# Performance work log

Hardware: AMD Instinct MI355X
Metric: run time of the kernel (lower is better)

## Reference

```python
import jax, jax.numpy as jnp
import numpy as np

HIDDEN = 1024
HEADS = 16
HEAD_DIM = HIDDEN // HEADS


def setup_inputs() -> dict:
    key = jax.random.key(0)
    ks = jax.random.split(key, 9)
    s = 1.0 / np.sqrt(HIDDEN)
    x = jax.random.normal(ks[0], (1, 4096, HIDDEN), dtype=jnp.float32)
    return {
        "x": x,
        "wq": jax.random.normal(ks[1], (HIDDEN, HIDDEN), dtype=jnp.float32) * s,
        "bq": jnp.zeros((HIDDEN,), dtype=jnp.float32),
        "wk": jax.random.normal(ks[2], (HIDDEN, HIDDEN), dtype=jnp.float32) * s,
        "bk": jnp.zeros((HIDDEN,), dtype=jnp.float32),
        "wv": jax.random.normal(ks[3], (HIDDEN, HIDDEN), dtype=jnp.float32) * s,
        "bv": jnp.zeros((HIDDEN,), dtype=jnp.float32),
        "wo": jax.random.normal(ks[4], (HIDDEN, HIDDEN), dtype=jnp.float32) * s,
        "bo": jnp.zeros((HIDDEN,), dtype=jnp.float32),
    }


def reference(x, wq, bq, wk, bk, wv, bv, wo, bo):
    B, S, D = x.shape
    H, Hd = HEADS, HEAD_DIM
    # projections (torch Linear: y = x @ W.T + b)
    q = (x @ wq.T + bq).reshape(B, S, H, Hd).transpose(0, 2, 1, 3)  # [B,H,S,Hd]
    k = (x @ wk.T + bk).reshape(B, S, H, Hd).transpose(0, 2, 1, 3)
    v = (x @ wv.T + bv).reshape(B, S, H, Hd).transpose(0, 2, 1, 3)
    scores = jnp.einsum("bhqd,bhkd->bhqk", q, k) / jnp.sqrt(jnp.float32(Hd))
    attn = jax.nn.softmax(scores, axis=-1)  # full [B,H,S,S] matrix, faithful to source
    out = jnp.einsum("bhqk,bhkd->bhqd", attn, v)  # [B,H,S,Hd]
    out = out.transpose(0, 2, 1, 3).reshape(B, S, D)
    return out @ wo.T + bo
```

## Files before the change

### kernel.cpp

```cpp
#include <hip/hip_runtime.h>
#include <stdint.h>

#define S 4096
#define D 1024
#define H 16
#define HD 64

#define QK_SCALE 0.18033688011112042f

typedef short short8  __attribute__((ext_vector_type(8)));
typedef float floatx4 __attribute__((ext_vector_type(4)));
typedef float floatx16 __attribute__((ext_vector_type(16)));

__device__ __forceinline__ unsigned short f2bf(float f) {
  union { float f; unsigned int i; } x; x.f = f;
  unsigned int r = x.i + 0x7FFFu + ((x.i >> 16) & 1u);
  return (unsigned short)(r >> 16);
}

#if defined(__has_builtin)
#if __has_builtin(__builtin_amdgcn_cvt_pk_bf16_f32)
#define HAVE_PK_BF16 1
#endif
#if __has_builtin(__builtin_amdgcn_exp2f)
#define HAVE_RAW_EXP2 1
#endif
#endif

__device__ __forceinline__ unsigned int pkbf(float a, float b) {
#ifdef HAVE_PK_BF16
  typedef __bf16 bf2_t __attribute__((ext_vector_type(2)));
  bf2_t t = __builtin_amdgcn_cvt_pk_bf16_f32(a, b);
  return __builtin_bit_cast(unsigned int, t);
#else
  return (unsigned int)f2bf(a) | ((unsigned int)f2bf(b) << 16);
#endif
}

__device__ __forceinline__ float fexp2(float x) {
#ifdef HAVE_RAW_EXP2
  return __builtin_amdgcn_exp2f(x);
#else
  return exp2f(x);
#endif
}

__device__ __forceinline__ void async16(const unsigned short* g, unsigned short* l) {
  __builtin_amdgcn_global_load_lds(
      (const __attribute__((address_space(1))) unsigned int*)g,
      (__attribute__((address_space(3))) unsigned int*)l, 16, 0, 0);
}

__global__ __launch_bounds__(256) void cvt_kernel(
    const float* __restrict__ x,  unsigned short* __restrict__ xb,
    const float* __restrict__ wq, unsigned short* __restrict__ wqb,
    const float* __restrict__ wk, unsigned short* __restrict__ wkb,
    const float* __restrict__ wv, unsigned short* __restrict__ wvb,
    const float* __restrict__ wo, unsigned short* __restrict__ wob,
    const float* __restrict__ bq, float* __restrict__ bqs)
{
  const int z = blockIdx.y;
  const float* s; unsigned short* d;
  float scale = 1.f;
  if (z < 4)       { s = x + (size_t)z * 1048576; d = xb + (size_t)z * 1048576; }
  else if (z == 4) { s = wq; d = wqb; scale = QK_SCALE; }
  else if (z == 5) { s = wk; d = wkb; }
  else if (z == 6) { s = wv; d = wvb; }
  else             { s = wo; d = wob; }
  const size_t i = ((size_t)blockIdx.x * 256 + threadIdx.x) * 4;
  float4 v = *reinterpret_cast<const float4*>(s + i);
  uint2 o;
  o.x = pkbf(v.x * scale, v.y * scale);
  o.y = pkbf(v.z * scale, v.w * scale);
  *reinterpret_cast<uint2*>(d + i) = o;
  if (z == 4 && blockIdx.x == 0) {
    const int t = threadIdx.x;
    #pragma unroll
    for (int j = 0; j < 4; ++j) bqs[t * 4 + j] = bq[t * 4 + j] * QK_SCALE;
  }
}

__global__ __launch_bounds__(256) void gemm_bt(
    const unsigned short* __restrict__ X,
    const unsigned short* __restrict__ W0, const float* __restrict__ B0, unsigned short* __restrict__ C0,
    const unsigned short* __restrict__ W1, const float* __restrict__ B1, unsigned short* __restrict__ C1,
    const unsigned short* __restrict__ W2, const float* __restrict__ B2, unsigned short* __restrict__ C2,
    float* __restrict__ Cf, unsigned short* __restrict__ VtOut)
{
  const unsigned short* W; const float* Bb; unsigned short* C;
  const int z = blockIdx.z;
  if (z == 0)      { W = W0; Bb = B0; C = C0; }
  else if (z == 1) { W = W1; Bb = B1; C = C1; }
  else             { W = W2; Bb = B2; C = C2; }

  const int bm = blockIdx.y, bn = blockIdx.x;
  const int tid  = threadIdx.x;
  const int lane = tid & 63, wave = tid >> 6;
  const int quad = lane >> 4, n16 = lane & 15;
  const int wm = (wave >> 1) * 64, wn = (wave & 1) * 64;

  __shared__ union {
    struct { unsigned short A[2][128 * 32]; unsigned short B[2][128 * 32]; } s;
    unsigned short T[64 * 136];
  } sm;

  floatx4 zero = {0.f, 0.f, 0.f, 0.f};
  floatx4 acc[4][4];
  #pragma unroll
  for (int i = 0; i < 4; ++i)
    #pragma unroll
    for (int j = 0; j < 4; ++j) acc[i][j] = zero;

  const int srow = 16 * wave + (lane >> 2);
  const int scol = (lane & 3) * 8;
  const unsigned short* XaL = X + (size_t)(bm * 128 + srow) * D + scol;
  const unsigned short* WaL = W + (size_t)(bn * 128 + srow) * D + scol;
  unsigned short* ldsA[2][2], * ldsB[2][2];
  #pragma unroll
  for (int sl = 0; sl < 2; ++sl) {
    ldsA[sl][0] = &sm.s.A[sl][(16 * wave) * 32];
    ldsA[sl][1] = &sm.s.A[sl][(64 + 16 * wave) * 32];
    ldsB[sl][0] = &sm.s.B[sl][(16 * wave) * 32];
    ldsB[sl][1] = &sm.s.B[sl][(64 + 16 * wave) * 32];
  }

  for (int k0 = 0; k0 < D; k0 += 64) {
    __syncthreads();
    #pragma unroll
    for (int sl = 0; sl < 2; ++sl) {
      async16(XaL + k0 + sl * 32, ldsA[sl][0]);
      async16(XaL + (size_t)64 * D + k0 + sl * 32, ldsA[sl][1]);
      async16(WaL + k0 + sl * 32, ldsB[sl][0]);
      async16(WaL + (size_t)64 * D + k0 + sl * 32, ldsB[sl][1]);
    }
    __syncthreads();

    #pragma unroll
    for (int sl = 0; sl < 2; ++sl) {
      short8 af[4], bfr[4];
      #pragma unroll
      for (int t = 0; t < 4; ++t) {
        af[t]  = *reinterpret_cast<const short8*>(&sm.s.A[sl][(wm + t * 16 + n16) * 32 + quad * 8]);
        bfr[t] = *reinterpret_cast<const short8*>(&sm.s.B[sl][(wn + t * 16 + n16) * 32 + quad * 8]);
      }
      #pragma unroll
      for (int tm = 0; tm < 4; ++tm)
        #pragma unroll
        for (int tn = 0; tn < 4; ++tn)
          acc[tm][tn] = __builtin_amdgcn_mfma_f32_16x16x32_bf16(af[tm], bfr[tn], acc[tm][tn], 0, 0, 0);
    }
  }

  if (z == 2 && VtOut) {
    #pragma unroll
    for (int p = 0; p < 2; ++p) {
      __syncthreads();
      if ((wn >> 6) == p) {
        #pragma unroll
        for (int tn = 0; tn < 4; ++tn) {
          const int col = bn * 128 + p * 64 + tn * 16 + n16;
          const float bias = Bb[col];
          #pragma unroll
          for (int tm = 0; tm < 4; ++tm) {
            uint2 w;
            w.x = pkbf(acc[tm][tn][0] + bias, acc[tm][tn][1] + bias);
            w.y = pkbf(acc[tm][tn][2] + bias, acc[tm][tn][3] + bias);
            *reinterpret_cast<uint2*>(&sm.T[(tn * 16 + n16) * 136 + wm + tm * 16 + quad * 4]) = w;
          }
        }
      }
      __syncthreads();
      {
        const int rl = tid >> 2, cc = (tid & 3) * 32;
        uint4 t0 = *reinterpret_cast<const uint4*>(&sm.T[rl * 136 + cc]);
        uint4 t1 = *reinterpret_cast<const uint4*>(&sm.T[rl * 136 + cc + 8]);
        uint4 t2 = *reinterpret_cast<const uint4*>(&sm.T[rl * 136 + cc + 16]);
        uint4 t3 = *reinterpret_cast<const uint4*>(&sm.T[rl * 136 + cc + 24]);
        uint4 n0, n1, n2, n3;
        n0.x = t0.x; n0.y = t0.y; n0.z = t1.x; n0.w = t1.y;
        n1.x = t0.z; n1.y = t0.w; n1.z = t1.z; n1.w = t1.w;
        n2.x = t2.x; n2.y = t2.y; n2.z = t3.x; n2.w = t3.y;
        n3.x = t2.z; n3.y = t2.w; n3.z = t3.z; n3.w = t3.w;
        const size_t go = (size_t)(bn * 128 + p * 64 + rl) * S + bm * 128 + cc;
        *reinterpret_cast<uint4*>(&VtOut[go])      = n0;
        *reinterpret_cast<uint4*>(&VtOut[go + 8])  = n1;
        *reinterpret_cast<uint4*>(&VtOut[go + 16]) = n2;
        *reinterpret_cast<uint4*>(&VtOut[go + 24]) = n3;
      }
    }
    return;
  }

  #pragma unroll
  for (int tn = 0; tn < 4; ++tn) {
    const int col = bn * 128 + wn + tn * 16 + n16;
    const float bias = Bb[col];
    #pragma unroll
    for (int tm = 0; tm < 4; ++tm) {
      const int rowb = bm * 128 + wm + tm * 16 + quad * 4;
      #pragma unroll
      for (int r = 0; r < 4; ++r) {
        const float v = acc[tm][tn][r] + bias;
        if (Cf) Cf[(size_t)(rowb + r) * D + col] = v;
        else    C[(size_t)(rowb + r) * D + col]  = f2bf(v);
      }
    }
  }
}

__global__ __launch_bounds__(256, 2) void attn(
    const unsigned short* __restrict__ Q,
    const unsigned short* __restrict__ K,
    const unsigned short* __restrict__ Vt,
    unsigned short* __restrict__ Op,
    float* __restrict__ Ls)
{
  const int h    = blockIdx.y;
  const int z    = blockIdx.z;
  const int q0   = blockIdx.x * 256;
  const int key0 = z * (S / 2);
  const int tid  = threadIdx.x;
  const int lane = tid & 63, wave = tid >> 6;
  const int l31 = lane & 31, h8 = lane >> 5;

  __shared__ unsigned short Ks[64 * 72];
  __shared__ unsigned short Vs[64 * 72];

  const int qA = q0 + wave * 64 + l31;
  const int qB = qA + 32;
  short8 qfA[4], qfB[4];
  #pragma unroll
  for (int ks = 0; ks < 4; ++ks) {
    qfA[ks] = *reinterpret_cast<const short8*>(Q + (size_t)qA * D + h * HD + ks * 16 + h8 * 8);
    qfB[ks] = *reinterpret_cast<const short8*>(Q + (size_t)qB * D + h * HD + ks * 16 + h8 * 8);
  }

  const short ONE = (short)0x3F80;
  short8 ones = {ONE, ONE, ONE, ONE, ONE, ONE, ONE, ONE};

  floatx16 oA0 = {}, oA1 = {}, oB0 = {}, oB1 = {};
  floatx16 accSA = {}, accSB = {};

  const int r1 = tid >> 2, c16 = (tid & 3) * 16;
  const unsigned short* Kbase = K  + (size_t)(key0 + r1) * D + h * HD + c16;
  const unsigned short* Vbase = Vt + (size_t)(h * HD + r1) * S + key0 + c16;

  uint4 ka, kb, va, vb;
  ka = *reinterpret_cast<const uint4*>(Kbase);
  kb = *reinterpret_cast<const uint4*>(Kbase + 8);
  va = *reinterpret_cast<const uint4*>(Vbase);
  vb = *reinterpret_cast<const uint4*>(Vbase + 8);

  const int NIT = (S / 2) / 64;
  for (int kt = 0; kt < NIT; ++kt) {
    __syncthreads();
    *reinterpret_cast<uint4*>(&Ks[r1 * 72 + c16])     = ka;
    *reinterpret_cast<uint4*>(&Ks[r1 * 72 + c16 + 8]) = kb;
    *reinterpret_cast<uint4*>(&Vs[r1 * 72 + c16])     = va;
    *reinterpret_cast<uint4*>(&Vs[r1 * 72 + c16 + 8]) = vb;
    __syncthreads();

    const int kn = (kt < NIT - 1) ? kt + 1 : kt;
    ka = *reinterpret_cast<const uint4*>(Kbase + (size_t)kn * 64 * D);
    kb = *reinterpret_cast<const uint4*>(Kbase + (size_t)kn * 64 * D + 8);
    va = *reinterpret_cast<const uint4*>(Vbase + kn * 64);
    vb = *reinterpret_cast<const uint4*>(Vbase + kn * 64 + 8);

    floatx16 sA0 = {}, sA1 = {}, sB0 = {}, sB1 = {};
    #pragma unroll
    for (int ks = 0; ks < 4; ++ks) {
      short8 a0 = *reinterpret_cast<const short8*>(&Ks[l31 * 72 + ks * 16 + h8 * 8]);
      short8 a1 = *reinterpret_cast<const short8*>(&Ks[(32 + l31) * 72 + ks * 16 + h8 * 8]);
      sA0 = __builtin_amdgcn_mfma_f32_32x32x16_bf16(a0, qfA[ks], sA0, 0, 0, 0);
      sA1 = __builtin_amdgcn_mfma_f32_32x32x16_bf16(a1, qfA[ks], sA1, 0, 0, 0);
      sB0 = __builtin_amdgcn_mfma_f32_32x32x16_bf16(a0, qfB[ks], sB0, 0, 0, 0);
      sB1 = __builtin_amdgcn_mfma_f32_32x32x16_bf16(a1, qfB[ks], sB1, 0, 0, 0);
    }

    #pragma unroll
    for (int r = 0; r < 16; ++r) {
      sA0[r] = fexp2(sA0[r]);
      sA1[r] = fexp2(sA1[r]);
      sB0[r] = fexp2(sB0[r]);
      sB1[r] = fexp2(sB1[r]);
    }

    short8 pbA[4], pbB[4];
    {
      unsigned int* ua = reinterpret_cast<unsigned int*>(pbA);
      unsigned int* ub = reinterpret_cast<unsigned int*>(pbB);
      #pragma unroll
      for (int i = 0; i < 8; ++i) {
        ua[i]     = pkbf(sA0[2 * i], sA0[2 * i + 1]);
        ua[8 + i] = pkbf(sA1[2 * i], sA1[2 * i + 1]);
        ub[i]     = pkbf(sB0[2 * i], sB0[2 * i + 1]);
        ub[8 + i] = pkbf(sB1[2 * i], sB1[2 * i + 1]);
      }
    }

    #pragma unroll
    for (int ks = 0; ks < 4; ++ks) {
      short8 va0 = *reinterpret_cast<const short8*>(&Vs[l31 * 72 + ks * 16 + h8 * 8]);
      short8 va1 = *reinterpret_cast<const short8*>(&Vs[(32 + l31) * 72 + ks * 16 + h8 * 8]);
      oA0 = __builtin_amdgcn_mfma_f32_32x32x16_bf16(va0, pbA[ks], oA0, 0, 0, 0);
      oA1 = __builtin_amdgcn_mfma_f32_32x32x16_bf16(va1, pbA[ks], oA1, 0, 0, 0);
      oB0 = __builtin_amdgcn_mfma_f32_32x32x16_bf16(va0, pbB[ks], oB0, 0, 0, 0);
      oB1 = __builtin_amdgcn_mfma_f32_32x32x16_bf16(va1, pbB[ks], oB1, 0, 0, 0);
      accSA = __builtin_amdgcn_mfma_f32_32x32x16_bf16(ones, pbA[ks], accSA, 0, 0, 0);
      accSB = __builtin_amdgcn_mfma_f32_32x32x16_bf16(ones, pbB[ks], accSB, 0, 0, 0);
    }
  }

  if (h8 == 0) {
    Ls[(size_t)z * S * H + qA * H + h] = accSA[0];
    Ls[(size_t)z * S * H + qB * H + h] = accSB[0];
  }

  unsigned short* obA = Op + (size_t)z * S * D + (size_t)qA * D + h * HD;
  unsigned short* obB = Op + (size_t)z * S * D + (size_t)qB * D + h * HD;
  #pragma unroll
  for (int rg = 0; rg < 4; ++rg) {
    uint2 w0, w1;
    w0.x = pkbf(oA0[rg * 4 + 0], oA0[rg * 4 + 1]);
    w0.y = pkbf(oA0[rg * 4 + 2], oA0[rg * 4 + 3]);
    w1.x = pkbf(oA1[rg * 4 + 0], oA1[rg * 4 + 1]);
    w1.y = pkbf(oA1[rg * 4 + 2], oA1[rg * 4 + 3]);
    *reinterpret_cast<uint2*>(&obA[rg * 8 + h8 * 4])      = w0;
    *reinterpret_cast<uint2*>(&obA[32 + rg * 8 + h8 * 4]) = w1;
    uint2 v0, v1;
    v0.x = pkbf(oB0[rg * 4 + 0], oB0[rg * 4 + 1]);
    v0.y = pkbf(oB0[rg * 4 + 2], oB0[rg * 4 + 3]);
    v1.x = pkbf(oB1[rg * 4 + 0], oB1[rg * 4 + 1]);
    v1.y = pkbf(oB1[rg * 4 + 2], oB1[rg * 4 + 3]);
    *reinterpret_cast<uint2*>(&obB[rg * 8 + h8 * 4])      = v0;
    *reinterpret_cast<uint2*>(&obB[32 + rg * 8 + h8 * 4]) = v1;
  }
}

__global__ __launch_bounds__(256) void combine(
    unsigned short* __restrict__ Op,
    const float* __restrict__ Ls)
{
  const size_t e8 = ((size_t)blockIdx.x * 256 + threadIdx.x) * 8;
  const int q = (int)(e8 >> 10);
  const int col = (int)(e8 & 1023);
  const int hh = col >> 6;
  const float l = Ls[q * H + hh] + Ls[S * H + q * H + hh];
  const float inv = 1.f / l;
  uint4 a = *reinterpret_cast<const uint4*>(Op + e8);
  uint4 b = *reinterpret_cast<const uint4*>(Op + (size_t)S * D + e8);
  uint4 r;
  const unsigned int* au = &a.x; const unsigned int* bu = &b.x; unsigned int* ru = &r.x;
  #pragma unroll
  for (int w = 0; w < 4; ++w) {
    union { unsigned int i; float f; } alo, ahi, blo, bhi;
    alo.i = au[w] << 16;          ahi.i = au[w] & 0xFFFF0000u;
    blo.i = bu[w] << 16;          bhi.i = bu[w] & 0xFFFF0000u;
    ru[w] = pkbf((alo.f + blo.f) * inv, (ahi.f + bhi.f) * inv);
  }
  *reinterpret_cast<uint4*>(Op + e8) = r;
}

extern "C" void kernel_launch(void* const* d_in, const int* in_sizes, int n_in,
                              void* d_out, int out_size, void* d_ws, size_t ws_size,
                              hipStream_t stream) {
  const float* x  = (const float*)d_in[0];
  const float* wq = (const float*)d_in[1];
  const float* bq = (const float*)d_in[2];
  const float* wk = (const float*)d_in[3];
  const float* bk = (const float*)d_in[4];
  const float* wv = (const float*)d_in[5];
  const float* bv = (const float*)d_in[6];
  const float* wo = (const float*)d_in[7];
  const float* bo = (const float*)d_in[8];
  float* out = (float*)d_out;

  unsigned short* ws = (unsigned short*)d_ws;
  const size_t SD = (size_t)S * D;
  const size_t DD = (size_t)D * D;
  unsigned short* xb  = ws;
  unsigned short* wqb = xb + SD;
  unsigned short* wkb = wqb + DD;
  unsigned short* wvb = wkb + DD;
  unsigned short* wob = wvb + DD;
  unsigned short* Qw  = wob + DD;
  unsigned short* Kw  = Qw + SD;
  unsigned short* Vtw = Kw + SD;
  unsigned short* Op  = Vtw + SD;
  float* Ls  = (float*)(Op + 2 * SD);
  float* bqs = Ls + 2 * (size_t)S * H;

  dim3 blk(256);
  cvt_kernel<<<dim3(1024, 8), blk, 0, stream>>>(x, xb, wq, wqb, wk, wkb, wv, wvb, wo, wob, bq, bqs);
  gemm_bt<<<dim3(D / 128, S / 128, 3), blk, 0, stream>>>(
      xb, wqb, bqs, Qw, wkb, bk, Kw, wvb, bv, nullptr, nullptr, Vtw);
  attn<<<dim3(S / 256, H, 2), blk, 0, stream>>>(Qw, Kw, Vtw, Op, Ls);
  combine<<<dim3(SD / (256 * 8)), blk, 0, stream>>>(Op, Ls);
  gemm_bt<<<dim3(D / 128, S / 128, 1), blk, 0, stream>>>(
      Op, wob, bo, nullptr, wob, bo, nullptr, wob, bo, nullptr, out, nullptr);
}
```

Baseline: 251.6 us.

## Fuse split-KV combine into output projection GEMM with 64-row tiles

Result: slower. 267.1 us (+6.2%).

```diff
diff --git a/kernel.cpp b/kernel.cpp
--- a/kernel.cpp
+++ b/kernel.cpp
@@ -43,6 +43,13 @@
 #else
   return exp2f(x);
 #endif
+}
+
+__device__ __forceinline__ unsigned int addpk(unsigned int a, unsigned int b, float inv) {
+  union { unsigned int i; float f; } alo, ahi, blo, bhi;
+  alo.i = a << 16;  ahi.i = a & 0xFFFF0000u;
+  blo.i = b << 16;  bhi.i = b & 0xFFFF0000u;
+  return pkbf((alo.f + blo.f) * inv, (ahi.f + bhi.f) * inv);
 }
 
 __device__ __forceinline__ void async16(const unsigned short* g, unsigned short* l) {
@@ -85,7 +92,7 @@
     const unsigned short* __restrict__ W0, const float* __restrict__ B0, unsigned short* __restrict__ C0,
     const unsigned short* __restrict__ W1, const float* __restrict__ B1, unsigned short* __restrict__ C1,
     const unsigned short* __restrict__ W2, const float* __restrict__ B2, unsigned short* __restrict__ C2,
-    float* __restrict__ Cf, unsigned short* __restrict__ VtOut)
+    unsigned short* __restrict__ VtOut)
 {
   const unsigned short* W; const float* Bb; unsigned short* C;
   const int z = blockIdx.z;
@@ -104,34 +111,21 @@
     unsigned short T[64 * 136];
   } sm;
 
-  floatx4 zero = {0.f, 0.f, 0.f, 0.f};
-  floatx4 acc[4][4];
-  #pragma unroll
-  for (int i = 0; i < 4; ++i)
-    #pragma unroll
-    for (int j = 0; j < 4; ++j) acc[i][j] = zero;
+  floatx4 acc[4][4] = {};
 
   const int srow = 16 * wave + (lane >> 2);
   const int scol = (lane & 3) * 8;
   const unsigned short* XaL = X + (size_t)(bm * 128 + srow) * D + scol;
   const unsigned short* WaL = W + (size_t)(bn * 128 + srow) * D + scol;
-  unsigned short* ldsA[2][2], * ldsB[2][2];
-  #pragma unroll
-  for (int sl = 0; sl < 2; ++sl) {
-    ldsA[sl][0] = &sm.s.A[sl][(16 * wave) * 32];
-    ldsA[sl][1] = &sm.s.A[sl][(64 + 16 * wave) * 32];
-    ldsB[sl][0] = &sm.s.B[sl][(16 * wave) * 32];
-    ldsB[sl][1] = &sm.s.B[sl][(64 + 16 * wave) * 32];
-  }
 
   for (int k0 = 0; k0 < D; k0 += 64) {
     __syncthreads();
     #pragma unroll
     for (int sl = 0; sl < 2; ++sl) {
-      async16(XaL + k0 + sl * 32, ldsA[sl][0]);
-      async16(XaL + (size_t)64 * D + k0 + sl * 32, ldsA[sl][1]);
-      async16(WaL + k0 + sl * 32, ldsB[sl][0]);
-      async16(WaL + (size_t)64 * D + k0 + sl * 32, ldsB[sl][1]);
+      async16(XaL + k0 + sl * 32, &sm.s.A[sl][(16 * wave) * 32]);
+      async16(XaL + (size_t)64 * D + k0 + sl * 32, &sm.s.A[sl][(64 + 16 * wave) * 32]);
+      async16(WaL + k0 + sl * 32, &sm.s.B[sl][(16 * wave) * 32]);
+      async16(WaL + (size_t)64 * D + k0 + sl * 32, &sm.s.B[sl][(64 + 16 * wave) * 32]);
     }
     __syncthreads();
 
@@ -199,11 +193,8 @@
     for (int tm = 0; tm < 4; ++tm) {
       const int rowb = bm * 128 + wm + tm * 16 + quad * 4;
       #pragma unroll
-      for (int r = 0; r < 4; ++r) {
-        const float v = acc[tm][tn][r] + bias;
-        if (Cf) Cf[(size_t)(rowb + r) * D + col] = v;
-        else    C[(size_t)(rowb + r) * D + col]  = f2bf(v);
-      }
+      for (int r = 0; r < 4; ++r)
+        C[(size_t)(rowb + r) * D + col] = f2bf(acc[tm][tn][r] + bias);
     }
   }
 }
@@ -337,28 +328,76 @@
   }
 }
 
-__global__ __launch_bounds__(256) void combine(
-    unsigned short* __restrict__ Op,
-    const float* __restrict__ Ls)
+__global__ __launch_bounds__(256) void gemm_out64(
+    const unsigned short* __restrict__ Op,
+    const float* __restrict__ Ls,
+    const unsigned short* __restrict__ Wo,
+    const float* __restrict__ bo,
+    float* __restrict__ out)
 {
-  const size_t e8 = ((size_t)blockIdx.x * 256 + threadIdx.x) * 8;
-  const int q = (int)(e8 >> 10);
-  const int col = (int)(e8 & 1023);
-  const int hh = col >> 6;
-  const float l = Ls[q * H + hh] + Ls[S * H + q * H + hh];
-  const float inv = 1.f / l;
-  uint4 a = *reinterpret_cast<const uint4*>(Op + e8);
-  uint4 b = *reinterpret_cast<const uint4*>(Op + (size_t)S * D + e8);
-  uint4 r;
-  const unsigned int* au = &a.x; const unsigned int* bu = &b.x; unsigned int* ru = &r.x;
+  const int bm = blockIdx.y, bn = blockIdx.x;
+  const int tid = threadIdx.x, lane = tid & 63, wave = tid >> 6;
+  const int quad = lane >> 4, n16 = lane & 15;
+  const int wm = (wave >> 1) * 32, wn = (wave & 1) * 64;
+
+  __shared__ unsigned short As[2][64 * 32];
+  __shared__ unsigned short Bs[2][128 * 32];
+
+  floatx4 acc[2][4] = {};
+
+  const int srow = 16 * wave + (lane >> 2);
+  const int scol = (lane & 3) * 8;
+  const int arow = bm * 64 + srow;
+  const unsigned short* A0 = Op + (size_t)arow * D + scol;
+  const unsigned short* A1 = A0 + (size_t)S * D;
+  const unsigned short* WaL = Wo + (size_t)(bn * 128 + srow) * D + scol;
+
+  for (int k0 = 0; k0 < D; k0 += 64) {
+    const int hh = k0 >> 6;
+    const float inv = 1.f / (Ls[arow * H + hh] + Ls[(size_t)S * H + arow * H + hh]);
+    __syncthreads();
+    #pragma unroll
+    for (int sl = 0; sl < 2; ++sl) {
+      uint4 a = *reinterpret_cast<const uint4*>(A0 + k0 + sl * 32);
+      uint4 b = *reinterpret_cast<const uint4*>(A1 + k0 + sl * 32);
+      uint4 c;
+      c.x = addpk(a.x, b.x, inv); c.y = addpk(a.y, b.y, inv);
+      c.z = addpk(a.z, b.z, inv); c.w = addpk(a.w, b.w, inv);
+      *reinterpret_cast<uint4*>(&As[sl][srow * 32 + scol]) = c;
+      async16(WaL + k0 + sl * 32, &Bs[sl][(16 * wave) * 32]);
+      async16(WaL + (size_t)64 * D + k0 + sl * 32, &Bs[sl][(64 + 16 * wave) * 32]);
+    }
+    __syncthreads();
+
+    #pragma unroll
+    for (int sl = 0; sl < 2; ++sl) {
+      short8 af[2], bfr[4];
+      #pragma unroll
+      for (int t = 0; t < 2; ++t)
+        af[t] = *reinterpret_cast<const short8*>(&As[sl][(wm + t * 16 + n16) * 32 + quad * 8]);
+      #pragma unroll
+      for (int t = 0; t < 4; ++t)
+        bfr[t] = *reinterpret_cast<const short8*>(&Bs[sl][(wn + t * 16 + n16) * 32 + quad * 8]);
+      #pragma unroll
+      for (int tm = 0; tm < 2; ++tm)
+        #pragma unroll
+        for (int tn = 0; tn < 4; ++tn)
+          acc[tm][tn] = __builtin_amdgcn_mfma_f32_16x16x32_bf16(af[tm], bfr[tn], acc[tm][tn], 0, 0, 0);
+    }
+  }
+
   #pragma unroll
-  for (int w = 0; w < 4; ++w) {
-    union { unsigned int i; float f; } alo, ahi, blo, bhi;
-    alo.i = au[w] << 16;          ahi.i = au[w] & 0xFFFF0000u;
-    blo.i = bu[w] << 16;          bhi.i = bu[w] & 0xFFFF0000u;
-    ru[w] = pkbf((alo.f + blo.f) * inv, (ahi.f + bhi.f) * inv);
-  }
-  *reinterpret_cast<uint4*>(Op + e8) = r;
+  for (int tn = 0; tn < 4; ++tn) {
+    const int col = bn * 128 + wn + tn * 16 + n16;
+    const float bias = bo[col];
+    #pragma unroll
+    for (int tm = 0; tm < 2; ++tm) {
+      const int rowb = bm * 64 + wm + tm * 16 + quad * 4;
+      #pragma unroll
+      for (int r = 0; r < 4; ++r)
+        out[(size_t)(rowb + r) * D + col] = acc[tm][tn][r] + bias;
+    }
+  }
 }
 
 extern "C" void kernel_launch(void* const* d_in, const int* in_sizes, int n_in,
@@ -393,9 +432,7 @@
   dim3 blk(256);
   cvt_kernel<<<dim3(1024, 8), blk, 0, stream>>>(x, xb, wq, wqb, wk, wkb, wv, wvb, wo, wob, bq, bqs);
   gemm_bt<<<dim3(D / 128, S / 128, 3), blk, 0, stream>>>(
-      xb, wqb, bqs, Qw, wkb, bk, Kw, wvb, bv, nullptr, nullptr, Vtw);
+      xb, wqb, bqs, Qw, wkb, bk, Kw, wvb, bv, nullptr, Vtw);
   attn<<<dim3(S / 256, H, 2), blk, 0, stream>>>(Qw, Kw, Vtw, Op, Ls);
-  combine<<<dim3(SD / (256 * 8)), blk, 0, stream>>>(Op, Ls);
-  gemm_bt<<<dim3(D / 128, S / 128, 1), blk, 0, stream>>>(
-      Op, wob, bo, nullptr, wob, bo, nullptr, wob, bo, nullptr, out, nullptr);
-}
+  gemm_out64<<<dim3(D / 128, S / 64), blk, 0, stream>>>(Op, Ls, wob, bo, out);
+}
```
